# Optimization experiments

Measured on AMD Instinct MI355X. Metric: run time of the kernel, lower is better.

## Reference

```python
import jax, jax.numpy as jnp
import numpy as np

M, N, DIM = 32, 32, 128
BATCH = 2048
NITER = 100
ALPHA = 0.3
SIGMA = max(M, N) / 2.0


def setup_inputs() -> dict:
    key = jax.random.key(0)
    k1, k2 = jax.random.split(key)
    x = jax.random.normal(k1, (BATCH, DIM), dtype=jnp.float32)
    weights = jax.random.normal(k2, (M * N, DIM), dtype=jnp.float32)
    # Grid locations exactly as in the torch module (meshgrid, ravel, transpose)
    xx, yy = np.meshgrid(np.linspace(0, M - 1, M), np.linspace(0, N - 1, N))
    locations = jnp.asarray(
        np.array((xx.ravel(), yy.ravel())).T.astype(np.int32)
    )  # [mn, 2]
    return {"x": x, "weights": weights, "locations": locations, "it": 5}


def reference(x, weights, locations, it):
    # --- BMU search: pairwise Euclidean distances weights [mn,d] vs x [b,d] ---
    # argmin over squared distances == argmin over cdist (sqrt is monotone)
    w2 = jnp.sum(weights * weights, axis=1)  # [mn]
    x2 = jnp.sum(x * x, axis=1)              # [b]
    d2 = w2[:, None] + x2[None, :] - 2.0 * (weights @ x.T)  # [mn, b]
    bmu_idx = jnp.argmin(d2, axis=0)         # [b]
    bmu_locs = locations[bmu_idx]            # [b, 2]

    # --- linearly decayed learning rate / neighbourhood width ---
    lr_decay = 1.0 - it / NITER
    alpha_op = ALPHA * lr_decay
    sigma_op = SIGMA * lr_decay

    # --- gaussian neighbourhood over grid distances: [mn, b] ---
    locf = locations.astype(jnp.float32)
    bmuf = bmu_locs.astype(jnp.float32)
    bmu_d2 = jnp.sum((locf[:, None, :] - bmuf[None, :, :]) ** 2, axis=2)  # [mn, b]
    lr_op = alpha_op * jnp.exp(-bmu_d2 / (sigma_op * sigma_op))           # [mn, b]

    # --- delta = sum_b lr_op[:, b] * (x[b] - w)  (algebraically reduced) ---
    # == lr_op @ x - rowsum(lr_op) * weights; avoids the [mn, b, d] intermediate
    delta = lr_op @ x - jnp.sum(lr_op, axis=1, keepdims=True) * weights  # [mn, d]
    return weights + delta
```

## Files before the change

### kernel.cpp

```cpp
#include <hip/hip_runtime.h>
#include <stdint.h>

#define DIM   128
#define MN    1024
#define BATCH 2048
#define ALPHA 0.3f
#define SIGMA 16.0f
#define LOG2E 1.44269504088896f

typedef _Float16 half8 __attribute__((ext_vector_type(8)));
typedef _Float16 half4 __attribute__((ext_vector_type(4)));
typedef float    floatx4 __attribute__((ext_vector_type(4)));


__global__ __launch_bounds__(256) void prep_kernel(
    const float* __restrict__ w, float* __restrict__ w2,
    _Float16* __restrict__ wh, _Float16* __restrict__ wl,
    float4* __restrict__ Sq)
{
  const int t = threadIdx.x;
  const int bid = blockIdx.x;
  if (bid < 8) {
    int idx = bid * 256 + t;
    int row = idx >> 1, half = idx & 1;
    int base = row * DIM + half * 64;
    float s = 0.f;
#pragma unroll
    for (int q = 0; q < 16; ++q) {
      float4 v = *reinterpret_cast<const float4*>(&w[base + q * 4]);
      s += v.x * v.x + v.y * v.y + v.z * v.z + v.w * v.w;
      half4 h, l;
      h[0] = (_Float16)v.x; l[0] = (_Float16)(v.x - (float)h[0]);
      h[1] = (_Float16)v.y; l[1] = (_Float16)(v.y - (float)h[1]);
      h[2] = (_Float16)v.z; l[2] = (_Float16)(v.z - (float)h[2]);
      h[3] = (_Float16)v.w; l[3] = (_Float16)(v.w - (float)h[3]);
      *reinterpret_cast<half4*>(&wh[base + q * 4]) = h;
      *reinterpret_cast<half4*>(&wl[base + q * 4]) = l;
    }
    s += __shfl_xor(s, 1);
    if (!half) w2[row] = s;
  } else {
    int i = (bid - 8) * 256 + t;
    Sq[i] = make_float4(0.f, 0.f, 0.f, 0.f);
  }
}

__global__ __launch_bounds__(1024) void bmu_scatter_kernel(
    const float* __restrict__ x, const float* __restrict__ w2,
    const _Float16* __restrict__ wh, const _Float16* __restrict__ wl,
    float* __restrict__ S, float* __restrict__ cnt)
{
  __shared__ unsigned long long kb[16][16];
  __shared__ unsigned long long fkey[16];

  const int t    = threadIdx.x;
  const int lane = t & 63;
  const int wv   = t >> 6;
  const int b0   = blockIdx.x * 16;
  const int r    = lane & 15;
  const int q    = lane >> 4;

  half8 Bh[4], Bl[4];
  {
    const float* xr = x + (b0 + r) * DIM + q * 8;
#pragma unroll
    for (int c = 0; c < 4; ++c) {
      float4 v0 = *reinterpret_cast<const float4*>(xr + c * 32);
      float4 v1 = *reinterpret_cast<const float4*>(xr + c * 32 + 4);
      float xs[8] = {v0.x, v0.y, v0.z, v0.w, v1.x, v1.y, v1.z, v1.w};
#pragma unroll
      for (int j = 0; j < 8; ++j) {
        _Float16 h = (_Float16)xs[j];
        Bh[c][j] = h;
        Bl[c][j] = (_Float16)(xs[j] - (float)h);
      }
    }
  }

  unsigned long long kmin = ~0ull;
#pragma unroll 2
  for (int ut = 0; ut < 4; ++ut) {
    const int u0 = wv * 64 + ut * 16;
    const _Float16* wrh = wh + (u0 + r) * DIM + q * 8;
    const _Float16* wrl = wl + (u0 + r) * DIM + q * 8;
    half8 Ah[4], Al[4];
#pragma unroll
    for (int c = 0; c < 4; ++c) {
      Ah[c] = *reinterpret_cast<const half8*>(wrh + c * 32);
      Al[c] = *reinterpret_cast<const half8*>(wrl + c * 32);
    }
    floatx4 acc = {0.f, 0.f, 0.f, 0.f};
#pragma unroll
    for (int c = 0; c < 4; ++c) {
      acc = __builtin_amdgcn_mfma_f32_16x16x32_f16(Ah[c], Bh[c], acc, 0, 0, 0);
      acc = __builtin_amdgcn_mfma_f32_16x16x32_f16(Ah[c], Bl[c], acc, 0, 0, 0);
      acc = __builtin_amdgcn_mfma_f32_16x16x32_f16(Al[c], Bh[c], acc, 0, 0, 0);
    }
    float4 w2q = *reinterpret_cast<const float4*>(&w2[u0 + q * 4]);
    float w2a[4] = {w2q.x, w2q.y, w2q.z, w2q.w};
#pragma unroll
    for (int i = 0; i < 4; ++i) {
      float s = w2a[i] - 2.0f * acc[i];
      unsigned int sb = __float_as_uint(s);
      sb ^= (sb >> 31) ? 0xFFFFFFFFu : 0x80000000u;
      unsigned long long key =
          ((unsigned long long)sb << 32) | (unsigned int)(u0 + q * 4 + i);
      if (key < kmin) kmin = key;
    }
  }
  unsigned long long o;
  o = __shfl_xor(kmin, 16); if (o < kmin) kmin = o;
  o = __shfl_xor(kmin, 32); if (o < kmin) kmin = o;
  if (lane < 16) kb[wv][r] = kmin;
  __syncthreads();
  if (t < 16) {
    unsigned long long m = kb[0][t];
#pragma unroll
    for (int k = 1; k < 16; ++k)
      if (kb[k][t] < m) m = kb[k][t];
    fkey[t] = m;
  }
  __syncthreads();

  if (t < 512) {
    int bl = t >> 5, cq = t & 31;
    unsigned int v = (unsigned int)fkey[bl];
    float4 xv = *reinterpret_cast<const float4*>(&x[(b0 + bl) * DIM + cq * 4]);
    float* Sv = S + v * DIM + cq * 4;
    unsafeAtomicAdd(&Sv[0], xv.x);
    unsafeAtomicAdd(&Sv[1], xv.y);
    unsafeAtomicAdd(&Sv[2], xv.z);
    unsafeAtomicAdd(&Sv[3], xv.w);
    if (cq == 0) unsafeAtomicAdd(&cnt[v], 1.0f);
  }
}

__global__ __launch_bounds__(512) void convfinal_kernel(
    const float* __restrict__ S, const float* __restrict__ cnt,
    const float* __restrict__ w, const int* __restrict__ itp,
    float* __restrict__ out)
{
  __shared__ float gxt[64], gyt[64];
  __shared__ float T1[4][32][4];
  __shared__ float Tcc[4][32];

  const int t   = threadIdx.x;
  const int q   = blockIdx.x >> 3;
  const int uxg = blockIdx.x & 7;
  const int ui  = t >> 7;
  const int ux  = uxg * 4 + ui;
  const int rem = t & 127;
  const int vy  = rem >> 2;
  const int j   = rem & 3;

  const float lr_decay = 1.0f - (float)itp[0] * 0.01f;
  const float alpha_op = ALPHA * lr_decay;
  const float sg       = SIGMA * lr_decay;
  const float c2       = -LOG2E / (sg * sg);

  if (t < 63) {
    float dd = (float)(t - 31);
    float g = __builtin_amdgcn_exp2f(c2 * dd * dd);
    gxt[t] = g;
    gyt[t] = alpha_op * g;
  }
  __syncthreads();

  {
    float a = 0.f, ac = 0.f;
    const float* Sp = S + (vy * 32) * DIM + q * 4 + j;
    const float* Cp = cnt + vy * 32;
#pragma unroll 8
    for (int vx = 0; vx < 32; ++vx) {
      float g = gxt[ux - vx + 31];
      a = fmaf(g, Sp[vx * DIM], a);
      if (j == 0) ac = fmaf(g, Cp[vx], ac);
    }
    T1[ui][vy][j] = a;
    if (j == 0) Tcc[ui][vy] = ac;
  }
  __syncthreads();

  {
    const int uy = vy;
    float d = 0.f, rs = 0.f;
#pragma unroll 8
    for (int v = 0; v < 32; ++v) {
      float g = gyt[uy - v + 31];
      d  = fmaf(g, T1[ui][v][j], d);
      rs = fmaf(g, Tcc[ui][v], rs);
    }
    int p = (uy * 32 + ux) * DIM + q * 4 + j;
    out[p] = w[p] * (1.0f - rs) + d;
  }
}

extern "C" void kernel_launch(void* const* d_in, const int* in_sizes, int n_in,
                              void* d_out, int out_size, void* d_ws, size_t ws_size,
                              hipStream_t stream) {
  const float* x   = (const float*)d_in[0];
  const float* w   = (const float*)d_in[1];
  const int*   itp = (const int*)d_in[3];
  float* out = (float*)d_out;

  char* ws = (char*)d_ws;
  float*     S   = (float*)ws;
  float*     cnt = (float*)(ws + 524288);
  float*     w2  = (float*)(ws + 528384);
  _Float16*  wh  = (_Float16*)(ws + 532480);
  _Float16*  wl  = (_Float16*)(ws + 794624);

  prep_kernel<<<137, 256, 0, stream>>>(w, w2, wh, wl, (float4*)S);
  bmu_scatter_kernel<<<128, 1024, 0, stream>>>(x, w2, wh, wl, S, cnt);
  convfinal_kernel<<<256, 512, 0, stream>>>(S, cnt, w, itp, out);
}
```

Before: 103.9 us.

## Fold weight prep into BMU kernel and bin into LDS in conv kernel

Removes the separate prep kernel: the BMU kernel now reads fp32 weights directly, splits them into hi/lo halves in registers and computes row norms with cross-lane shuffles. The global float atomics that scattered x into S and cnt are replaced by a compact BMU key buffer. Each convolution block rebuilds its 4-column slice of the per-node sums and counts with LDS atomics. This cuts one launch, the workspace zeroing and the contended global atomics. In exchange, x is re-read by every convolution block, the weights are reconverted per block, and the count plane sees heavy LDS atomic contention.

```diff
diff --git a/kernel.cpp b/kernel.cpp
--- a/kernel.cpp
+++ b/kernel.cpp
@@ -9,49 +9,14 @@
 #define LOG2E 1.44269504088896f
 
 typedef _Float16 half8 __attribute__((ext_vector_type(8)));
-typedef _Float16 half4 __attribute__((ext_vector_type(4)));
 typedef float    floatx4 __attribute__((ext_vector_type(4)));
 
 
-__global__ __launch_bounds__(256) void prep_kernel(
-    const float* __restrict__ w, float* __restrict__ w2,
-    _Float16* __restrict__ wh, _Float16* __restrict__ wl,
-    float4* __restrict__ Sq)
-{
-  const int t = threadIdx.x;
-  const int bid = blockIdx.x;
-  if (bid < 8) {
-    int idx = bid * 256 + t;
-    int row = idx >> 1, half = idx & 1;
-    int base = row * DIM + half * 64;
-    float s = 0.f;
-#pragma unroll
-    for (int q = 0; q < 16; ++q) {
-      float4 v = *reinterpret_cast<const float4*>(&w[base + q * 4]);
-      s += v.x * v.x + v.y * v.y + v.z * v.z + v.w * v.w;
-      half4 h, l;
-      h[0] = (_Float16)v.x; l[0] = (_Float16)(v.x - (float)h[0]);
-      h[1] = (_Float16)v.y; l[1] = (_Float16)(v.y - (float)h[1]);
-      h[2] = (_Float16)v.z; l[2] = (_Float16)(v.z - (float)h[2]);
-      h[3] = (_Float16)v.w; l[3] = (_Float16)(v.w - (float)h[3]);
-      *reinterpret_cast<half4*>(&wh[base + q * 4]) = h;
-      *reinterpret_cast<half4*>(&wl[base + q * 4]) = l;
-    }
-    s += __shfl_xor(s, 1);
-    if (!half) w2[row] = s;
-  } else {
-    int i = (bid - 8) * 256 + t;
-    Sq[i] = make_float4(0.f, 0.f, 0.f, 0.f);
-  }
-}
-
-__global__ __launch_bounds__(1024) void bmu_scatter_kernel(
-    const float* __restrict__ x, const float* __restrict__ w2,
-    const _Float16* __restrict__ wh, const _Float16* __restrict__ wl,
-    float* __restrict__ S, float* __restrict__ cnt)
+__global__ __launch_bounds__(1024) void bmu_kernel(
+    const float* __restrict__ x, const float* __restrict__ w,
+    unsigned int* __restrict__ keys)
 {
   __shared__ unsigned long long kb[16][16];
-  __shared__ unsigned long long fkey[16];
 
   const int t    = threadIdx.x;
   const int lane = t & 63;
@@ -81,14 +46,28 @@
 #pragma unroll 2
   for (int ut = 0; ut < 4; ++ut) {
     const int u0 = wv * 64 + ut * 16;
-    const _Float16* wrh = wh + (u0 + r) * DIM + q * 8;
-    const _Float16* wrl = wl + (u0 + r) * DIM + q * 8;
     half8 Ah[4], Al[4];
+    float w2p = 0.f;
+    {
+      const float* wr = w + (u0 + r) * DIM + q * 8;
 #pragma unroll
-    for (int c = 0; c < 4; ++c) {
-      Ah[c] = *reinterpret_cast<const half8*>(wrh + c * 32);
-      Al[c] = *reinterpret_cast<const half8*>(wrl + c * 32);
+      for (int c = 0; c < 4; ++c) {
+        float4 v0 = *reinterpret_cast<const float4*>(wr + c * 32);
+        float4 v1 = *reinterpret_cast<const float4*>(wr + c * 32 + 4);
+        float wsb[8] = {v0.x, v0.y, v0.z, v0.w, v1.x, v1.y, v1.z, v1.w};
+#pragma unroll
+        for (int j = 0; j < 8; ++j) {
+          float vv = wsb[j];
+          w2p = fmaf(vv, vv, w2p);
+          _Float16 h = (_Float16)vv;
+          Ah[c][j] = h;
+          Al[c][j] = (_Float16)(vv - (float)h);
+        }
+      }
     }
+    w2p += __shfl_xor(w2p, 16);
+    w2p += __shfl_xor(w2p, 32);
+
     floatx4 acc = {0.f, 0.f, 0.f, 0.f};
 #pragma unroll
     for (int c = 0; c < 4; ++c) {
@@ -96,11 +75,10 @@
       acc = __builtin_amdgcn_mfma_f32_16x16x32_f16(Ah[c], Bl[c], acc, 0, 0, 0);
       acc = __builtin_amdgcn_mfma_f32_16x16x32_f16(Al[c], Bh[c], acc, 0, 0, 0);
     }
-    float4 w2q = *reinterpret_cast<const float4*>(&w2[u0 + q * 4]);
-    float w2a[4] = {w2q.x, w2q.y, w2q.z, w2q.w};
 #pragma unroll
     for (int i = 0; i < 4; ++i) {
-      float s = w2a[i] - 2.0f * acc[i];
+      float w2v = __shfl(w2p, q * 4 + i);
+      float s = w2v - 2.0f * acc[i];
       unsigned int sb = __float_as_uint(s);
       sb ^= (sb >> 31) ? 0xFFFFFFFFu : 0x80000000u;
       unsigned long long key =
@@ -118,28 +96,17 @@
 #pragma unroll
     for (int k = 1; k < 16; ++k)
       if (kb[k][t] < m) m = kb[k][t];
-    fkey[t] = m;
-  }
-  __syncthreads();
-
-  if (t < 512) {
-    int bl = t >> 5, cq = t & 31;
-    unsigned int v = (unsigned int)fkey[bl];
-    float4 xv = *reinterpret_cast<const float4*>(&x[(b0 + bl) * DIM + cq * 4]);
-    float* Sv = S + v * DIM + cq * 4;
-    unsafeAtomicAdd(&Sv[0], xv.x);
-    unsafeAtomicAdd(&Sv[1], xv.y);
-    unsafeAtomicAdd(&Sv[2], xv.z);
-    unsafeAtomicAdd(&Sv[3], xv.w);
-    if (cq == 0) unsafeAtomicAdd(&cnt[v], 1.0f);
+    keys[b0 + t] = (unsigned int)m;
   }
 }
 
-__global__ __launch_bounds__(512) void convfinal_kernel(
-    const float* __restrict__ S, const float* __restrict__ cnt,
+#define PLANE 1064
+__global__ __launch_bounds__(512) void convgather_kernel(
+    const float* __restrict__ x, const unsigned int* __restrict__ keys,
     const float* __restrict__ w, const int* __restrict__ itp,
     float* __restrict__ out)
 {
+  __shared__ float bin[4 * PLANE + 32 * 33];
   __shared__ float gxt[64], gyt[64];
   __shared__ float T1[4][32][4];
   __shared__ float Tcc[4][32];
@@ -147,17 +114,13 @@
   const int t   = threadIdx.x;
   const int q   = blockIdx.x >> 3;
   const int uxg = blockIdx.x & 7;
-  const int ui  = t >> 7;
-  const int ux  = uxg * 4 + ui;
-  const int rem = t & 127;
-  const int vy  = rem >> 2;
-  const int j   = rem & 3;
+
+  for (int i = t; i < 4 * PLANE + 32 * 33; i += 512) bin[i] = 0.f;
 
   const float lr_decay = 1.0f - (float)itp[0] * 0.01f;
   const float alpha_op = ALPHA * lr_decay;
   const float sg       = SIGMA * lr_decay;
   const float c2       = -LOG2E / (sg * sg);
-
   if (t < 63) {
     float dd = (float)(t - 31);
     float g = __builtin_amdgcn_exp2f(c2 * dd * dd);
@@ -166,14 +129,35 @@
   }
   __syncthreads();
 
+#pragma unroll
+  for (int s = 0; s < 4; ++s) {
+    int b = s * 512 + t;
+    unsigned int v = keys[b];
+    int vy = v >> 5, vx = v & 31;
+    float4 xv = *reinterpret_cast<const float4*>(&x[b * DIM + q * 4]);
+    int base = vy * 33 + vx;
+    atomicAdd(&bin[0 * PLANE + base], xv.x);
+    atomicAdd(&bin[1 * PLANE + base], xv.y);
+    atomicAdd(&bin[2 * PLANE + base], xv.z);
+    atomicAdd(&bin[3 * PLANE + base], xv.w);
+    atomicAdd(&bin[4 * PLANE + base], 1.0f);
+  }
+  __syncthreads();
+
+  const int ui  = t >> 7;
+  const int ux  = uxg * 4 + ui;
+  const int rem = t & 127;
+  const int vy  = rem >> 2;
+  const int j   = rem & 3;
+
   {
     float a = 0.f, ac = 0.f;
-    const float* Sp = S + (vy * 32) * DIM + q * 4 + j;
-    const float* Cp = cnt + vy * 32;
+    const float* Sp = bin + j * PLANE + vy * 33;
+    const float* Cp = bin + 4 * PLANE + vy * 33;
 #pragma unroll 8
     for (int vx = 0; vx < 32; ++vx) {
       float g = gxt[ux - vx + 31];
-      a = fmaf(g, Sp[vx * DIM], a);
+      a = fmaf(g, Sp[vx], a);
       if (j == 0) ac = fmaf(g, Cp[vx], ac);
     }
     T1[ui][vy][j] = a;
@@ -203,14 +187,8 @@
   const int*   itp = (const int*)d_in[3];
   float* out = (float*)d_out;
 
-  char* ws = (char*)d_ws;
-  float*     S   = (float*)ws;
-  float*     cnt = (float*)(ws + 524288);
-  float*     w2  = (float*)(ws + 528384);
-  _Float16*  wh  = (_Float16*)(ws + 532480);
-  _Float16*  wl  = (_Float16*)(ws + 794624);
+  unsigned int* keys = (unsigned int*)d_ws;
 
-  prep_kernel<<<137, 256, 0, stream>>>(w, w2, wh, wl, (float4*)S);
-  bmu_scatter_kernel<<<128, 1024, 0, stream>>>(x, w2, wh, wl, S, cnt);
-  convfinal_kernel<<<256, 512, 0, stream>>>(S, cnt, w, itp, out);
+  bmu_kernel<<<128, 1024, 0, stream>>>(x, w, keys);
+  convgather_kernel<<<256, 512, 0, stream>>>(x, keys, w, itp, out);
 }
```

Result: faster. 95.17 us (-8.4%).
